# Kernel tuning notes

Hardware: AMD Instinct MI355X
Metric: run time of the kernel (lower is better)

Reference implementation:

```python
import jax, jax.numpy as jnp
import numpy as np
from jax.ops import segment_sum, segment_max

N, E, H, C = 20000, 320000, 4, 128
G, NF, EF, GF = 1024, 9, 4, 50
EPS = 1e-5
NEG_SLOPE = 0.2


def setup_inputs() -> dict:
    key = jax.random.key(0)
    ks = jax.random.split(key, 16)
    inp = {
        'x': jax.random.normal(ks[0], (N, NF), jnp.float32),
        'edge_attr': jax.random.normal(ks[1], (E, EF), jnp.float32),
        'global_feat': jax.random.normal(ks[2], (G, GF), jnp.float32),
        'Wl1': jax.random.normal(ks[3], (NF, H * C), jnp.float32) * 0.1,
        'Wr1': jax.random.normal(ks[4], (NF, H * C), jnp.float32) * 0.1,
        'We1': jax.random.normal(ks[5], (EF, H * C), jnp.float32) * 0.1,
        'att1': jax.random.normal(ks[6], (H, C), jnp.float32) * 0.1,
        'b1': jax.random.normal(ks[7], (H * C,), jnp.float32) * 0.01,
        'gamma1': jnp.ones((H * C,), jnp.float32),
        'beta1': jnp.zeros((H * C,), jnp.float32),
        'mean1': jnp.zeros((H * C,), jnp.float32),
        'var1': jnp.ones((H * C,), jnp.float32),
        'Wl2': jax.random.normal(ks[8], (H * C, H * C), jnp.float32) * 0.05,
        'Wr2': jax.random.normal(ks[9], (H * C, H * C), jnp.float32) * 0.05,
        'We2': jax.random.normal(ks[10], (EF, H * C), jnp.float32) * 0.1,
        'att2': jax.random.normal(ks[11], (H, C), jnp.float32) * 0.1,
        'b2': jax.random.normal(ks[12], (H * C,), jnp.float32) * 0.01,
        'gamma2': jnp.ones((H * C,), jnp.float32),
        'beta2': jnp.zeros((H * C,), jnp.float32),
        'mean2': jnp.zeros((H * C,), jnp.float32),
        'var2': jnp.ones((H * C,), jnp.float32),
        'fc1_w': jax.random.normal(ks[13], (H * C + GF, C), jnp.float32) * 0.05,
        'fc1_b': jnp.zeros((C,), jnp.float32),
        'fc2_w': jax.random.normal(ks[14], (C, 1), jnp.float32) * 0.1,
        'fc2_b': jnp.zeros((1,), jnp.float32),
        'edge_index': jax.random.randint(ks[15], (2, E), 0, N, jnp.int32),
        'batch': jnp.sort(jax.random.randint(jax.random.fold_in(key, 99), (N,), 0, G, jnp.int32)),
    }
    return inp


def gatv2_layer(x, src, dst, ea, Wl, Wr, We, att, bias):
    # PyG GATv2Conv: add self-loops with fill_value='mean' edge_attr
    n = x.shape[0]
    loop = jnp.arange(n, dtype=src.dtype)
    deg = segment_sum(jnp.ones((src.shape[0],), x.dtype), dst, num_segments=n)
    ea_mean = segment_sum(ea, dst, num_segments=n) / jnp.clip(deg, 1.0)[:, None]
    s = jnp.concatenate([src, loop])
    d = jnp.concatenate([dst, loop])
    eat = jnp.concatenate([ea, ea_mean], axis=0)
    xl = (x @ Wl).reshape(n, H, C)  # source transform
    xr = (x @ Wr).reshape(n, H, C)  # target transform
    ee = (eat @ We).reshape(-1, H, C)
    e = jax.nn.leaky_relu(xl[s] + xr[d] + ee, NEG_SLOPE)  # [E+N, H, C]
    logits = jnp.einsum('ehc,hc->eh', e, att)  # [E+N, H]
    m = segment_max(logits, d, num_segments=n)  # stable segment softmax
    ex = jnp.exp(logits - m[d])
    alpha = ex / segment_sum(ex, d, num_segments=n)[d]
    out = segment_sum(alpha[..., None] * xl[s], d, num_segments=n)  # [N, H, C]
    return out.reshape(n, H * C) + bias


def batch_norm(x, g, b, mu, var):
    return (x - mu) * jax.lax.rsqrt(var + EPS) * g + b


def reference(x, edge_attr, global_feat, Wl1, Wr1, We1, att1, b1, gamma1, beta1, mean1, var1,
              Wl2, Wr2, We2, att2, b2, gamma2, beta2, mean2, var2,
              fc1_w, fc1_b, fc2_w, fc2_b, edge_index, batch):
    src, dst = edge_index[0], edge_index[1]
    h = jax.nn.relu(batch_norm(gatv2_layer(x, src, dst, edge_attr, Wl1, Wr1, We1, att1, b1),
                               gamma1, beta1, mean1, var1))
    h = jax.nn.relu(batch_norm(gatv2_layer(h, src, dst, edge_attr, Wl2, Wr2, We2, att2, b2),
                               gamma2, beta2, mean2, var2))
    cnt = segment_sum(jnp.ones((h.shape[0],), h.dtype), batch, num_segments=G)
    pooled = segment_sum(h, batch, num_segments=G) / jnp.clip(cnt, 1.0)[:, None]  # [G, H*C]
    z = jnp.concatenate([pooled, global_feat], axis=1)
    z = jax.nn.relu(z @ fc1_w + fc1_b)
    return (z @ fc2_w + fc2_b).squeeze()
```

## Files before the change

kernel.cpp:

```cpp
#include <hip/hip_runtime.h>
#include <hip/hip_bf16.h>

#define Nn 20000
#define Ee 320000
#define Hh 4
#define Cc 128
#define HC 512
#define Gg 1024
#define NFt 9
#define EFt 4
#define GFt 50
#define EPSf 1e-5f
#define SLOPE 0.2f
#define NWAVES 4096

typedef __attribute__((ext_vector_type(8))) short bf16x8;
typedef __attribute__((ext_vector_type(4))) float f32x4;
typedef __attribute__((ext_vector_type(2))) float f32x2;
typedef __attribute__((ext_vector_type(4))) unsigned ui32x4;

typedef const __attribute__((address_space(1))) unsigned char* gp1_t;
typedef __attribute__((address_space(3))) unsigned char* lp3_t;
__device__ __forceinline__ void gload16(const void* g, void* l) {
    __builtin_amdgcn_global_load_lds((gp1_t)g, (lp3_t)l, 16, 0, 0);
}

__device__ __forceinline__ float bf2f(short s) {
    return __uint_as_float(((unsigned)(unsigned short)s) << 16);
}
__device__ __forceinline__ float rfl(float v) {
    return __uint_as_float(__builtin_amdgcn_readfirstlane(__float_as_uint(v)));
}

__device__ __forceinline__ f32x2 pkfma(f32x2 a, f32x2 b, f32x2 c) {
    f32x2 d;
    asm("v_pk_fma_f32 %0, %1, %2, %3" : "=v"(d) : "v"(a), "v"(b), "v"(c));
    return d;
}
__device__ __forceinline__ f32x2 pkadd(f32x2 a, f32x2 b) {
    f32x2 d;
    asm("v_pk_add_f32 %0, %1, %2" : "=v"(d) : "v"(a), "v"(b));
    return d;
}
__device__ __forceinline__ f32x2 pkmul(f32x2 a, f32x2 b) {
    f32x2 d;
    asm("v_pk_mul_f32 %0, %1, %2" : "=v"(d) : "v"(a), "v"(b));
    return d;
}

__global__ __launch_bounds__(256) void k_setup(
    const int* __restrict__ dst, int* __restrict__ deg, int* __restrict__ rank,
    const int* __restrict__ batch, int* __restrict__ gofs,
    const float* __restrict__ Wl2, const float* __restrict__ Wr2,
    __hip_bfloat16* __restrict__ Wt,
    const float* __restrict__ x, const float* __restrict__ Wl1,
    const float* __restrict__ Wr1, __hip_bfloat16* __restrict__ xl,
    __hip_bfloat16* __restrict__ xr) {
    __shared__ float tile[64][65];
    int b = blockIdx.x, t = threadIdx.x;
    if (b < 1250) {
        int e = b * 256 + t;
        if (e < Ee) rank[e] = atomicAdd(&deg[dst[e]], 1);
    } else if (b < 1329) {
        int i = (b - 1250) * 256 + t;
        if (i >= Nn) return;
        int bb = batch[i];
        if (i == 0) {
            for (int g = 0; g <= bb; ++g) gofs[g] = 0;
        } else {
            int bp = batch[i - 1];
            for (int g = bp + 1; g <= bb; ++g) gofs[g] = i;
        }
        if (i == Nn - 1) {
            for (int g = bb + 1; g <= Gg; ++g) gofs[g] = Nn;
        }
    } else if (b < 1457) {
        int tid = b - 1329;
        int tc = (tid >> 3) * 64;
        int tk = (tid & 7) * 64;
        int lc = t & 63, lr = t >> 6;
        const float* W = (tc < 512) ? Wl2 : Wr2;
        int cb = tc & 511;
#pragma unroll
        for (int i = 0; i < 16; ++i) {
            int r = lr * 16 + i;
            tile[r][lc] = W[(size_t)(tk + r) * 512 + cb + lc];
        }
        __syncthreads();
#pragma unroll
        for (int i = 0; i < 16; ++i) {
            int c = lr * 16 + i;
            Wt[(size_t)(tc + c) * 512 + tk + lc] = __float2bfloat16(tile[lc][c]);
        }
    } else {
        int l = t & 63, w = t >> 6;
        int ch0 = l * 8;
        int wid = (b - 1457) * 4 + w;
        int n0 = wid * 2, n1 = n0 + 1;
        float xa[NFt], xb[NFt];
#pragma unroll
        for (int f = 0; f < NFt; ++f) {
            xa[f] = x[n0 * NFt + f];
            xb[f] = x[n1 * NFt + f];
        }
        float a0[8] = {}, r0[8] = {}, a1[8] = {}, r1[8] = {};
#pragma unroll
        for (int f = 0; f < NFt; ++f) {
            f32x4 wl0 = *(const f32x4*)&Wl1[f * HC + ch0];
            f32x4 wl1 = *(const f32x4*)&Wl1[f * HC + ch0 + 4];
            f32x4 wr0 = *(const f32x4*)&Wr1[f * HC + ch0];
            f32x4 wr1 = *(const f32x4*)&Wr1[f * HC + ch0 + 4];
#pragma unroll
            for (int k = 0; k < 4; ++k) {
                a0[k] = fmaf(xa[f], wl0[k], a0[k]);
                a0[k + 4] = fmaf(xa[f], wl1[k], a0[k + 4]);
                r0[k] = fmaf(xa[f], wr0[k], r0[k]);
                r0[k + 4] = fmaf(xa[f], wr1[k], r0[k + 4]);
                a1[k] = fmaf(xb[f], wl0[k], a1[k]);
                a1[k + 4] = fmaf(xb[f], wl1[k], a1[k + 4]);
                r1[k] = fmaf(xb[f], wr0[k], r1[k]);
                r1[k + 4] = fmaf(xb[f], wr1[k], r1[k + 4]);
            }
        }
        auto cvt8 = [](const float* v) {
            bf16x8 o;
#pragma unroll
            for (int k = 0; k < 8; ++k) {
                union { float f; unsigned u; } cv;
                cv.f = v[k];
                unsigned r = (cv.u + 0x7fff + ((cv.u >> 16) & 1)) >> 16;
                o[k] = (short)r;
            }
            return o;
        };
        *(bf16x8*)(xl + (size_t)n0 * HC + ch0) = cvt8(a0);
        *(bf16x8*)(xr + (size_t)n0 * HC + ch0) = cvt8(r0);
        *(bf16x8*)(xl + (size_t)n1 * HC + ch0) = cvt8(a1);
        *(bf16x8*)(xr + (size_t)n1 * HC + ch0) = cvt8(r1);
    }
}

__global__ void k_scan(const int* __restrict__ deg, int* __restrict__ rowptr) {
    __shared__ int sums[1024];
    int t = threadIdx.x;
    const int n = Nn;
    int chunk = (n + 1023) / 1024;
    int start = t * chunk;
    int lim = min(start + chunk, n);
    int s = 0;
    for (int i = start; i < lim; ++i) s += deg[i];
    sums[t] = s;
    __syncthreads();
    for (int off = 1; off < 1024; off <<= 1) {
        int v = (t >= off) ? sums[t - off] : 0;
        __syncthreads();
        sums[t] += v;
        __syncthreads();
    }
    int run = (t == 0) ? 0 : sums[t - 1];
    for (int i = start; i < lim; ++i) { rowptr[i] = run; run += deg[i]; }
    if (t == 1023) rowptr[n] = sums[1023];
}

__global__ void k_scatter(const int* __restrict__ src, const int* __restrict__ dst,
                          const float* __restrict__ ea, const int* __restrict__ rowptr,
                          const int* __restrict__ rank, int* __restrict__ csr_src,
                          float4* __restrict__ ea_s) {
    int e = blockIdx.x * 256 + threadIdx.x;
    if (e >= Ee) return;
    int pos = rowptr[dst[e]] + rank[e];
    csr_src[pos] = src[e];
    ea_s[pos] = ((const float4*)ea)[e];
}

__global__ __launch_bounds__(256) void k_gemm_mfma(const short* __restrict__ Abf,
                                                   const short* __restrict__ Bt,
                                                   __hip_bfloat16* __restrict__ xl,
                                                   __hip_bfloat16* __restrict__ xr, int M) {
    __shared__ short As[128 * 32];
    __shared__ short Bs[128 * 32];
    int tid = threadIdx.x;
    int l = tid & 63;
    int wid = tid >> 6;
    int bm0 = blockIdx.x * 128;
    int bn0 = blockIdx.y * 128;
    int wr = (wid >> 1) * 64;
    int wc = (wid & 1) * 64;
    f32x4 acc[4][4] = {};

    int srow = l >> 2;
    int skoff = ((l & 3) ^ ((l >> 3) & 3)) * 8;
    int rk = (((l >> 4) ^ (l >> 1)) & 3) * 8;

    for (int k0 = 0; k0 < 512; k0 += 32) {
        {
            int c = wid;
            long row = min(bm0 + c * 16 + srow, M - 1);
            gload16(Abf + row * 512 + k0 + skoff, &As[c * 512]);
            int col = bn0 + c * 16 + srow;
            gload16(Bt + (size_t)col * 512 + k0 + skoff, &Bs[c * 512]);
            c = wid + 4;
            row = min(bm0 + c * 16 + srow, M - 1);
            gload16(Abf + row * 512 + k0 + skoff, &As[c * 512]);
            col = bn0 + c * 16 + srow;
            gload16(Bt + (size_t)col * 512 + k0 + skoff, &Bs[c * 512]);
        }
        asm volatile("s_waitcnt vmcnt(0)" ::: "memory");
        __syncthreads();
        bf16x8 af[4], bfr[4];
#pragma unroll
        for (int m = 0; m < 4; ++m)
            af[m] = *(const bf16x8*)&As[(wr + m * 16 + (l & 15)) * 32 + rk];
#pragma unroll
        for (int n = 0; n < 4; ++n)
            bfr[n] = *(const bf16x8*)&Bs[(wc + n * 16 + (l & 15)) * 32 + rk];
#pragma unroll
        for (int m = 0; m < 4; ++m)
#pragma unroll
            for (int n = 0; n < 4; ++n)
                acc[m][n] = __builtin_amdgcn_mfma_f32_16x16x32_bf16(af[m], bfr[n],
                                                                    acc[m][n], 0, 0, 0);
        __syncthreads();
    }
    __hip_bfloat16* dst = (bn0 < 512) ? xl : xr;
    int cb = bn0 & 511;
#pragma unroll
    for (int m = 0; m < 4; ++m) {
#pragma unroll
        for (int n = 0; n < 4; ++n) {
            int col = cb + wc + n * 16 + (l & 15);
#pragma unroll
            for (int r = 0; r < 4; ++r) {
                int row = bm0 + wr + m * 16 + (l >> 4) * 4 + r;
                if (row < M) dst[(size_t)row * 512 + col] = __float2bfloat16(acc[m][n][r]);
            }
        }
    }
}

__global__ __launch_bounds__(256) void k_fused_attn(
    const __hip_bfloat16* __restrict__ xl, const __hip_bfloat16* __restrict__ xr,
    const float* __restrict__ We, const float* __restrict__ att,
    const int* __restrict__ rowptr, const int* __restrict__ csr_src,
    const float4* __restrict__ ea_s, const float* __restrict__ bias,
    const float* __restrict__ gamma, const float* __restrict__ beta,
    const float* __restrict__ mean, const float* __restrict__ var,
    __hip_bfloat16* __restrict__ hout) {
    int l = threadIdx.x & 63;
    int wid = __builtin_amdgcn_readfirstlane(blockIdx.x * 4 + (threadIdx.x >> 6));
    int ch0 = l * 8;
    int nA = (int)(((long)wid * Nn) / NWAVES);
    int nB = (int)(((long)(wid + 1) * Nn) / NWAVES);

    f32x2 wee2[4][4], ar2[4];
#pragma unroll
    for (int f = 0; f < 4; ++f) {
        f32x4 w0 = *(const f32x4*)&We[f * HC + ch0];
        f32x4 w1 = *(const f32x4*)&We[f * HC + ch0 + 4];
        wee2[f][0] = (f32x2){w0.x, w0.y};
        wee2[f][1] = (f32x2){w0.z, w0.w};
        wee2[f][2] = (f32x2){w1.x, w1.y};
        wee2[f][3] = (f32x2){w1.z, w1.w};
    }
    {
        f32x4 a0 = *(const f32x4*)&att[ch0];
        f32x4 a1 = *(const f32x4*)&att[ch0 + 4];
        ar2[0] = (f32x2){a0.x, a0.y};
        ar2[1] = (f32x2){a0.z, a0.w};
        ar2[2] = (f32x2){a1.x, a1.y};
        ar2[3] = (f32x2){a1.z, a1.w};
    }
    float S[8], O[8];
    {
        f32x4 bi0 = *(const f32x4*)&bias[ch0], bi1 = *(const f32x4*)&bias[ch0 + 4];
        f32x4 ga0 = *(const f32x4*)&gamma[ch0], ga1 = *(const f32x4*)&gamma[ch0 + 4];
        f32x4 be0 = *(const f32x4*)&beta[ch0], be1 = *(const f32x4*)&beta[ch0 + 4];
        f32x4 me0 = *(const f32x4*)&mean[ch0], me1 = *(const f32x4*)&mean[ch0 + 4];
        f32x4 va0 = *(const f32x4*)&var[ch0], va1 = *(const f32x4*)&var[ch0 + 4];
#pragma unroll
        for (int k = 0; k < 8; ++k) {
            float bik = (k < 4) ? bi0[k] : bi1[k - 4];
            float gak = (k < 4) ? ga0[k] : ga1[k - 4];
            float bek = (k < 4) ? be0[k] : be1[k - 4];
            float mek = (k < 4) ? me0[k] : me1[k - 4];
            float vak = (k < 4) ? va0[k] : va1[k - 4];
            S[k] = gak * rsqrtf(vak + EPSf);
            O[k] = (bik - mek) * S[k] + bek;
        }
    }

    for (int n = nA; n < nB; ++n) {
        f32x2 rr2[4];
        {
            ui32x4 ru = *(const ui32x4*)(xr + (size_t)n * HC + ch0);
#pragma unroll
            for (int j = 0; j < 4; ++j) {
                unsigned u = ru[j];
                rr2[j] = (f32x2){__uint_as_float(u << 16),
                                 __uint_as_float(u & 0xffff0000u)};
            }
        }
        int start = __builtin_amdgcn_readfirstlane(rowptr[n]);
        int nedge = __builtin_amdgcn_readfirstlane(rowptr[n + 1]) - start;
        int last = start + nedge - 1;

        float m = -1e30f, den = 0.f;
        f32x2 acc2[4] = {};
        float es0 = 0.f, es1 = 0.f, es2 = 0.f, es3 = 0.f;

        struct Chunk {
            int s[4];
            float e[4][4];
            bf16x8 x[4];
        };

        auto accum4 = [&](const Chunk& c, const float* ex) {
#pragma unroll
            for (int i = 0; i < 4; ++i) {
                f32x2 esp = (f32x2){ex[i], ex[i]};
                ui32x4 xu = *(const ui32x4*)&c.x[i];
#pragma unroll
                for (int j = 0; j < 4; ++j) {
                    unsigned u = xu[j];
                    f32x2 xv = (f32x2){__uint_as_float(u << 16),
                                       __uint_as_float(u & 0xffff0000u)};
                    acc2[j] = pkfma(esp, xv, acc2[j]);
                }
            }
        };

        auto step = [&](Chunk& cur, Chunk& nxt, int base) {
#pragma unroll
            for (int i = 0; i < 4; ++i) {
                int idx = __builtin_amdgcn_readfirstlane(min(start + base + 4 + i, last));
                nxt.s[i] = __builtin_amdgcn_readfirstlane(csr_src[idx]);
                float4 v = ea_s[idx];
                nxt.e[i][0] = rfl(v.x); nxt.e[i][1] = rfl(v.y);
                nxt.e[i][2] = rfl(v.z); nxt.e[i][3] = rfl(v.w);
            }
#pragma unroll
            for (int i = 0; i < 4; ++i)
                nxt.x[i] = *(const bf16x8*)(xl + (size_t)nxt.s[i] * HC + ch0);

#pragma unroll
            for (int i = 0; i < 4; ++i) {
                if (base + i < nedge) {
                    es0 += cur.e[i][0]; es1 += cur.e[i][1];
                    es2 += cur.e[i][2]; es3 += cur.e[i][3];
                }
            }

            float p[4];
#pragma unroll
            for (int i = 0; i < 4; ++i) {
                ui32x4 xu = *(const ui32x4*)&cur.x[i];
                f32x2 es0p = (f32x2){cur.e[i][0], cur.e[i][0]};
                f32x2 es1p = (f32x2){cur.e[i][1], cur.e[i][1]};
                f32x2 es2p = (f32x2){cur.e[i][2], cur.e[i][2]};
                f32x2 es3p = (f32x2){cur.e[i][3], cur.e[i][3]};
                f32x2 plin = (f32x2){0.f, 0.f}, pabs = (f32x2){0.f, 0.f};
#pragma unroll
                for (int j = 0; j < 4; ++j) {
                    unsigned u = xu[j];
                    f32x2 xv = (f32x2){__uint_as_float(u << 16),
                                       __uint_as_float(u & 0xffff0000u)};
                    f32x2 z = pkadd(xv, rr2[j]);
                    z = pkfma(es0p, wee2[0][j], z);
                    z = pkfma(es1p, wee2[1][j], z);
                    z = pkfma(es2p, wee2[2][j], z);
                    z = pkfma(es3p, wee2[3][j], z);
                    f32x2 za = (f32x2){fabsf(z.x), fabsf(z.y)};
                    plin = pkfma(ar2[j], z, plin);
                    pabs = pkfma(ar2[j], za, pabs);
                }
                p[i] = 0.6f * (plin.x + plin.y) + 0.4f * (pabs.x + pabs.y);
            }
#pragma unroll
            for (int off = 8; off; off >>= 1) {
                p[0] += __shfl_xor(p[0], off);
                p[1] += __shfl_xor(p[1], off);
                p[2] += __shfl_xor(p[2], off);
                p[3] += __shfl_xor(p[3], off);
            }
#pragma unroll
            for (int i = 1; i < 4; ++i)
                if (base + i >= nedge) p[i] = -1e30f;

            float pmax = fmaxf(fmaxf(p[0], p[1]), fmaxf(p[2], p[3]));
            float ex[4];
            if (__all(pmax <= m + 8.f)) {
                ex[0] = __expf(p[0] - m); ex[1] = __expf(p[1] - m);
                ex[2] = __expf(p[2] - m); ex[3] = __expf(p[3] - m);
                den += ex[0] + ex[1] + ex[2] + ex[3];
                accum4(cur, ex);
            } else {
                float mn = fmaxf(m, pmax);
                float sc = __expf(m - mn);
                ex[0] = __expf(p[0] - mn); ex[1] = __expf(p[1] - mn);
                ex[2] = __expf(p[2] - mn); ex[3] = __expf(p[3] - mn);
                den = den * sc + ex[0] + ex[1] + ex[2] + ex[3];
                f32x2 scs = (f32x2){sc, sc};
#pragma unroll
                for (int j = 0; j < 4; ++j) acc2[j] = pkmul(acc2[j], scs);
                accum4(cur, ex);
                m = mn;
            }
        };

        if (nedge > 0) {
            Chunk A, B;
#pragma unroll
            for (int i = 0; i < 4; ++i) {
                int idx = __builtin_amdgcn_readfirstlane(min(start + i, last));
                A.s[i] = __builtin_amdgcn_readfirstlane(csr_src[idx]);
                float4 v = ea_s[idx];
                A.e[i][0] = rfl(v.x); A.e[i][1] = rfl(v.y);
                A.e[i][2] = rfl(v.z); A.e[i][3] = rfl(v.w);
            }
#pragma unroll
            for (int i = 0; i < 4; ++i)
                A.x[i] = *(const bf16x8*)(xl + (size_t)A.s[i] * HC + ch0);

            int base = 0;
            for (;;) {
                step(A, B, base);
                base += 4;
                if (base >= nedge) break;
                step(B, A, base);
                base += 4;
                if (base >= nedge) break;
            }
        }

        {
            float dv = (float)max(nedge, 1);
            float e0 = es0 / dv, e1 = es1 / dv, e2 = es2 / dv, e3 = es3 / dv;
            ui32x4 xu = *(const ui32x4*)(xl + (size_t)n * HC + ch0);
            f32x2 es0p = (f32x2){e0, e0}, es1p = (f32x2){e1, e1};
            f32x2 es2p = (f32x2){e2, e2}, es3p = (f32x2){e3, e3};
            f32x2 plin = (f32x2){0.f, 0.f}, pabs = (f32x2){0.f, 0.f};
            f32x2 xv2[4];
#pragma unroll
            for (int j = 0; j < 4; ++j) {
                unsigned u = xu[j];
                xv2[j] = (f32x2){__uint_as_float(u << 16),
                                 __uint_as_float(u & 0xffff0000u)};
                f32x2 z = pkadd(xv2[j], rr2[j]);
                z = pkfma(es0p, wee2[0][j], z);
                z = pkfma(es1p, wee2[1][j], z);
                z = pkfma(es2p, wee2[2][j], z);
                z = pkfma(es3p, wee2[3][j], z);
                f32x2 za = (f32x2){fabsf(z.x), fabsf(z.y)};
                plin = pkfma(ar2[j], z, plin);
                pabs = pkfma(ar2[j], za, pabs);
            }
            float pi = 0.6f * (plin.x + plin.y) + 0.4f * (pabs.x + pabs.y);
#pragma unroll
            for (int off = 8; off; off >>= 1) pi += __shfl_xor(pi, off);
            float mn = fmaxf(m, pi);
            float sc = __expf(m - mn);
            float ex = __expf(pi - mn);
            den = den * sc + ex;
            f32x2 scs = (f32x2){sc, sc};
            f32x2 exs = (f32x2){ex, ex};
#pragma unroll
            for (int j = 0; j < 4; ++j)
                acc2[j] = pkfma(exs, xv2[j], pkmul(acc2[j], scs));
        }

        float iden = 1.f / den;
        float aflat[8] = {acc2[0].x, acc2[0].y, acc2[1].x, acc2[1].y,
                          acc2[2].x, acc2[2].y, acc2[3].x, acc2[3].y};
        bf16x8 ob;
#pragma unroll
        for (int k = 0; k < 8; ++k) {
            float v = fmaxf(fmaf(aflat[k] * iden, S[k], O[k]), 0.f);
            union { float f; unsigned u; } cv;
            cv.f = v;
            unsigned r = (cv.u + 0x7fff + ((cv.u >> 16) & 1)) >> 16;
            ob[k] = (short)r;
        }
        *(bf16x8*)(hout + (size_t)n * HC + ch0) = ob;
    }
}

__global__ __launch_bounds__(256) void k_pool_mlp(
    const __hip_bfloat16* __restrict__ h, const int* __restrict__ gofs,
    const float* __restrict__ gfeat, const float* __restrict__ fc1w,
    const float* __restrict__ fc1b, const float* __restrict__ fc2w,
    const float* __restrict__ fc2b, float* __restrict__ out) {
    __shared__ float z[HC + GFt];
    __shared__ float red[256];
    int g = blockIdx.x, t = threadIdx.x;
    int s = gofs[g], e = gofs[g + 1];
    float a0 = 0.f, a1 = 0.f;
    for (int r = s; r < e; ++r) {
        ushort2 v = ((const ushort2*)(h + (size_t)r * HC))[t];
        a0 += bf2f((short)v.x);
        a1 += bf2f((short)v.y);
    }
    float ic = (e > s) ? 1.f / (float)(e - s) : 0.f;
    z[2 * t] = a0 * ic;
    z[2 * t + 1] = a1 * ic;
    if (t < GFt) z[HC + t] = gfeat[g * GFt + t];
    __syncthreads();
    int c = t & 127, half = t >> 7;
    float acc = (half == 0) ? fc1b[c] : 0.f;
    int j0 = half * 281, j1 = j0 + 281;
    for (int j = j0; j < j1; ++j) acc += z[j] * fc1w[j * 128 + c];
    red[t] = acc;
    __syncthreads();
    if (t < 128) {
        float a = red[t] + red[t + 128];
        red[t] = fmaxf(a, 0.f) * fc2w[t];
    }
    __syncthreads();
    for (int off = 64; off; off >>= 1) {
        if (t < off) red[t] += red[t + off];
        __syncthreads();
    }
    if (t == 0) out[g] = red[0] + fc2b[0];
}

extern "C" void kernel_launch(void* const* d_in, const int* in_sizes, int n_in,
                              void* d_out, int out_size, void* d_ws, size_t ws_size,
                              hipStream_t stream) {
    const float* x = (const float*)d_in[0];
    const float* ea = (const float*)d_in[1];
    const float* gfeat = (const float*)d_in[2];
    const float* Wl1 = (const float*)d_in[3];
    const float* Wr1 = (const float*)d_in[4];
    const float* We1 = (const float*)d_in[5];
    const float* att1 = (const float*)d_in[6];
    const float* b1 = (const float*)d_in[7];
    const float* gamma1 = (const float*)d_in[8];
    const float* beta1 = (const float*)d_in[9];
    const float* mean1 = (const float*)d_in[10];
    const float* var1 = (const float*)d_in[11];
    const float* Wl2 = (const float*)d_in[12];
    const float* Wr2 = (const float*)d_in[13];
    const float* We2 = (const float*)d_in[14];
    const float* att2 = (const float*)d_in[15];
    const float* b2 = (const float*)d_in[16];
    const float* gamma2 = (const float*)d_in[17];
    const float* beta2 = (const float*)d_in[18];
    const float* mean2 = (const float*)d_in[19];
    const float* var2 = (const float*)d_in[20];
    const float* fc1w = (const float*)d_in[21];
    const float* fc1b = (const float*)d_in[22];
    const float* fc2w = (const float*)d_in[23];
    const float* fc2b = (const float*)d_in[24];
    const int* eidx = (const int*)d_in[25];
    const int* batch = (const int*)d_in[26];
    float* out = (float*)d_out;

    const int* srcp = eidx;
    const int* dstp = eidx + Ee;

    char* p = (char*)d_ws;
    auto alloc = [&](size_t bytes) -> char* {
        char* r = p;
        p += (bytes + 255) & ~(size_t)255;
        return r;
    };
    __hip_bfloat16* xl = (__hip_bfloat16*)alloc((size_t)Nn * HC * 2);
    __hip_bfloat16* xr = (__hip_bfloat16*)alloc((size_t)Nn * HC * 2);
    __hip_bfloat16* h_bf = (__hip_bfloat16*)alloc((size_t)Nn * HC * 2);
    int* deg = (int*)alloc((size_t)Nn * 4);
    int* rank = (int*)alloc((size_t)Ee * 4);
    int* rowptr = (int*)alloc((size_t)(Nn + 1) * 4);
    int* csr_src = (int*)alloc((size_t)Ee * 4);
    float4* ea_s = (float4*)alloc((size_t)Ee * 16);
    int* gofs = (int*)alloc((size_t)(Gg + 1) * 4);
    __hip_bfloat16* Wt = (__hip_bfloat16*)alloc((size_t)1024 * 512 * 2);

    hipMemsetAsync(deg, 0, (size_t)Nn * 4, stream);

    k_setup<<<1457 + 2500, 256, 0, stream>>>(dstp, deg, rank, batch, gofs, Wl2, Wr2,
                                             Wt, x, Wl1, Wr1, xl, xr);
    k_scan<<<1, 1024, 0, stream>>>(deg, rowptr);
    k_scatter<<<(Ee + 255) / 256, 256, 0, stream>>>(srcp, dstp, ea, rowptr, rank,
                                                    csr_src, ea_s);

    k_fused_attn<<<NWAVES / 4, 256, 0, stream>>>(xl, xr, We1, att1, rowptr, csr_src,
                                                 ea_s, b1, gamma1, beta1, mean1, var1,
                                                 h_bf);

    k_gemm_mfma<<<dim3((Nn + 127) / 128, 8), 256, 0, stream>>>(
        (const short*)h_bf, (const short*)Wt, xl, xr, Nn);
    k_fused_attn<<<NWAVES / 4, 256, 0, stream>>>(xl, xr, We2, att2, rowptr, csr_src,
                                                 ea_s, b2, gamma2, beta2, mean2, var2,
                                                 h_bf);

    k_pool_mlp<<<Gg, 256, 0, stream>>>(h_bf, gofs, gfeat, fc1w, fc1b, fc2w, fc2b, out);
}
```

Measured before the change: 324.7 us.

## Assign one wave per node and stage edge metadata via lane bpermute

The attention kernel now launches one wave per destination node instead of a fixed pool of persistent waves that loop over node ranges. Each wave loads up to 64 edge source indices and edge attributes cooperatively, one per lane, and broadcasts them with ds_bpermute. This replaces the per-edge scalar readfirstlane loads. Gather addresses become 32-bit byte offsets, and the BN scale/offset is computed after the loop. The aim is to cut serialized scalar load latency and improve latency hiding across many waves, at the cost of more launched waves and recomputing per-wave constants for every node.

```diff
diff --git a/kernel.cpp b/kernel.cpp
--- a/kernel.cpp
+++ b/kernel.cpp
@@ -12,7 +12,6 @@
 #define GFt 50
 #define EPSf 1e-5f
 #define SLOPE 0.2f
-#define NWAVES 4096
 
 typedef __attribute__((ext_vector_type(8))) short bf16x8;
 typedef __attribute__((ext_vector_type(4))) float f32x4;
@@ -28,9 +27,6 @@
 __device__ __forceinline__ float bf2f(short s) {
     return __uint_as_float(((unsigned)(unsigned short)s) << 16);
 }
-__device__ __forceinline__ float rfl(float v) {
-    return __uint_as_float(__builtin_amdgcn_readfirstlane(__float_as_uint(v)));
-}
 
 __device__ __forceinline__ f32x2 pkfma(f32x2 a, f32x2 b, f32x2 c) {
     f32x2 d;
@@ -46,6 +42,12 @@
     f32x2 d;
     asm("v_pk_mul_f32 %0, %1, %2" : "=v"(d) : "v"(a), "v"(b));
     return d;
+}
+__device__ __forceinline__ int bperm(int byteaddr, int v) {
+    return __builtin_amdgcn_ds_bpermute(byteaddr, v);
+}
+__device__ __forceinline__ float bpermf(int byteaddr, float v) {
+    return __int_as_float(__builtin_amdgcn_ds_bpermute(byteaddr, __float_as_int(v)));
 }
 
 __global__ __launch_bounds__(256) void k_setup(
@@ -246,13 +248,14 @@
     const float* __restrict__ gamma, const float* __restrict__ beta,
     const float* __restrict__ mean, const float* __restrict__ var,
     __hip_bfloat16* __restrict__ hout) {
+    int n = blockIdx.x * 4 + (threadIdx.x >> 6);
+    if (n >= Nn) return;
     int l = threadIdx.x & 63;
-    int wid = __builtin_amdgcn_readfirstlane(blockIdx.x * 4 + (threadIdx.x >> 6));
     int ch0 = l * 8;
-    int nA = (int)(((long)wid * Nn) / NWAVES);
-    int nB = (int)(((long)(wid + 1) * Nn) / NWAVES);
-
-    f32x2 wee2[4][4], ar2[4];
+    const unsigned char* xlb = (const unsigned char*)xl;
+    int choff = ch0 * 2;
+
+    f32x2 wee2[4][4], ar2[4], rr2[4];
 #pragma unroll
     for (int f = 0; f < 4; ++f) {
         f32x4 w0 = *(const f32x4*)&We[f * HC + ch0];
@@ -270,55 +273,108 @@
         ar2[2] = (f32x2){a1.x, a1.y};
         ar2[3] = (f32x2){a1.z, a1.w};
     }
-    float S[8], O[8];
     {
-        f32x4 bi0 = *(const f32x4*)&bias[ch0], bi1 = *(const f32x4*)&bias[ch0 + 4];
-        f32x4 ga0 = *(const f32x4*)&gamma[ch0], ga1 = *(const f32x4*)&gamma[ch0 + 4];
-        f32x4 be0 = *(const f32x4*)&beta[ch0], be1 = *(const f32x4*)&beta[ch0 + 4];
-        f32x4 me0 = *(const f32x4*)&mean[ch0], me1 = *(const f32x4*)&mean[ch0 + 4];
-        f32x4 va0 = *(const f32x4*)&var[ch0], va1 = *(const f32x4*)&var[ch0 + 4];
-#pragma unroll
-        for (int k = 0; k < 8; ++k) {
-            float bik = (k < 4) ? bi0[k] : bi1[k - 4];
-            float gak = (k < 4) ? ga0[k] : ga1[k - 4];
-            float bek = (k < 4) ? be0[k] : be1[k - 4];
-            float mek = (k < 4) ? me0[k] : me1[k - 4];
-            float vak = (k < 4) ? va0[k] : va1[k - 4];
-            S[k] = gak * rsqrtf(vak + EPSf);
-            O[k] = (bik - mek) * S[k] + bek;
-        }
-    }
-
-    for (int n = nA; n < nB; ++n) {
-        f32x2 rr2[4];
-        {
-            ui32x4 ru = *(const ui32x4*)(xr + (size_t)n * HC + ch0);
+        ui32x4 ru = *(const ui32x4*)(xr + (size_t)n * HC + ch0);
+#pragma unroll
+        for (int j = 0; j < 4; ++j) {
+            unsigned u = ru[j];
+            rr2[j] = (f32x2){__uint_as_float(u << 16), __uint_as_float(u & 0xffff0000u)};
+        }
+    }
+
+    int start = __builtin_amdgcn_readfirstlane(rowptr[n]);
+    int nedge = __builtin_amdgcn_readfirstlane(rowptr[n + 1]) - start;
+
+    float m = -1e30f, den = 0.f;
+    f32x2 acc2[4] = {};
+    float esl0 = 0.f, esl1 = 0.f, esl2 = 0.f, esl3 = 0.f;
+
+    struct Chunk {
+        float e[4][4];
+        bf16x8 x[4];
+    };
+
+    for (int mb = 0; mb < nedge; mb += 64) {
+        int cnt = min(64, nedge - mb);
+        int msrc = 0;
+        float4 mea = make_float4(0.f, 0.f, 0.f, 0.f);
+        if (l < cnt) {
+            msrc = csr_src[start + mb + l];
+            mea = ea_s[start + mb + l];
+        }
+        esl0 += mea.x; esl1 += mea.y; esl2 += mea.z; esl3 += mea.w;
+
+        auto fetch = [&](Chunk& C, int fb) {
 #pragma unroll
             for (int j = 0; j < 4; ++j) {
-                unsigned u = ru[j];
-                rr2[j] = (f32x2){__uint_as_float(u << 16),
-                                 __uint_as_float(u & 0xffff0000u)};
-            }
-        }
-        int start = __builtin_amdgcn_readfirstlane(rowptr[n]);
-        int nedge = __builtin_amdgcn_readfirstlane(rowptr[n + 1]) - start;
-        int last = start + nedge - 1;
-
-        float m = -1e30f, den = 0.f;
-        f32x2 acc2[4] = {};
-        float es0 = 0.f, es1 = 0.f, es2 = 0.f, es3 = 0.f;
-
-        struct Chunk {
-            int s[4];
-            float e[4][4];
-            bf16x8 x[4];
+                int ba = min(fb + j, cnt - 1) * 4;
+                int sj = bperm(ba, msrc);
+                C.e[j][0] = bpermf(ba, mea.x);
+                C.e[j][1] = bpermf(ba, mea.y);
+                C.e[j][2] = bpermf(ba, mea.z);
+                C.e[j][3] = bpermf(ba, mea.w);
+                unsigned voff = ((unsigned)sj << 10) + choff;
+                C.x[j] = *(const bf16x8*)(xlb + voff);
+            }
         };
 
-        auto accum4 = [&](const Chunk& c, const float* ex) {
+        auto compute = [&](const Chunk& C, int base) {
+            float p[4];
+#pragma unroll
+            for (int i = 0; i < 4; ++i) {
+                ui32x4 xu = *(const ui32x4*)&C.x[i];
+                f32x2 e0p = (f32x2){C.e[i][0], C.e[i][0]};
+                f32x2 e1p = (f32x2){C.e[i][1], C.e[i][1]};
+                f32x2 e2p = (f32x2){C.e[i][2], C.e[i][2]};
+                f32x2 e3p = (f32x2){C.e[i][3], C.e[i][3]};
+                f32x2 plin = (f32x2){0.f, 0.f}, pabs = (f32x2){0.f, 0.f};
+#pragma unroll
+                for (int j = 0; j < 4; ++j) {
+                    unsigned u = xu[j];
+                    f32x2 xv = (f32x2){__uint_as_float(u << 16),
+                                       __uint_as_float(u & 0xffff0000u)};
+                    f32x2 z = pkadd(xv, rr2[j]);
+                    z = pkfma(e0p, wee2[0][j], z);
+                    z = pkfma(e1p, wee2[1][j], z);
+                    z = pkfma(e2p, wee2[2][j], z);
+                    z = pkfma(e3p, wee2[3][j], z);
+                    f32x2 za = (f32x2){fabsf(z.x), fabsf(z.y)};
+                    plin = pkfma(ar2[j], z, plin);
+                    pabs = pkfma(ar2[j], za, pabs);
+                }
+                p[i] = 0.6f * (plin.x + plin.y) + 0.4f * (pabs.x + pabs.y);
+            }
+#pragma unroll
+            for (int off = 8; off; off >>= 1) {
+                p[0] += __shfl_xor(p[0], off);
+                p[1] += __shfl_xor(p[1], off);
+                p[2] += __shfl_xor(p[2], off);
+                p[3] += __shfl_xor(p[3], off);
+            }
+#pragma unroll
+            for (int i = 1; i < 4; ++i)
+                if (base + i >= cnt) p[i] = -1e30f;
+
+            float pmax = fmaxf(fmaxf(p[0], p[1]), fmaxf(p[2], p[3]));
+            float ex[4];
+            float mloc = m;
+            if (!__all(pmax <= mloc + 8.f)) {
+                float mn = fmaxf(mloc, pmax);
+                float sc = __expf(mloc - mn);
+                den *= sc;
+                f32x2 scs = (f32x2){sc, sc};
+#pragma unroll
+                for (int j = 0; j < 4; ++j) acc2[j] = pkmul(acc2[j], scs);
+                m = mn;
+                mloc = mn;
+            }
+            ex[0] = __expf(p[0] - mloc); ex[1] = __expf(p[1] - mloc);
+            ex[2] = __expf(p[2] - mloc); ex[3] = __expf(p[3] - mloc);
+            den += ex[0] + ex[1] + ex[2] + ex[3];
 #pragma unroll
             for (int i = 0; i < 4; ++i) {
                 f32x2 esp = (f32x2){ex[i], ex[i]};
-                ui32x4 xu = *(const ui32x4*)&c.x[i];
+                ui32x4 xu = *(const ui32x4*)&C.x[i];
 #pragma unroll
                 for (int j = 0; j < 4; ++j) {
                     unsigned u = xu[j];
@@ -329,159 +385,88 @@
             }
         };
 
-        auto step = [&](Chunk& cur, Chunk& nxt, int base) {
-#pragma unroll
-            for (int i = 0; i < 4; ++i) {
-                int idx = __builtin_amdgcn_readfirstlane(min(start + base + 4 + i, last));
-                nxt.s[i] = __builtin_amdgcn_readfirstlane(csr_src[idx]);
-                float4 v = ea_s[idx];
-                nxt.e[i][0] = rfl(v.x); nxt.e[i][1] = rfl(v.y);
-                nxt.e[i][2] = rfl(v.z); nxt.e[i][3] = rfl(v.w);
-            }
-#pragma unroll
-            for (int i = 0; i < 4; ++i)
-                nxt.x[i] = *(const bf16x8*)(xl + (size_t)nxt.s[i] * HC + ch0);
-
-#pragma unroll
-            for (int i = 0; i < 4; ++i) {
-                if (base + i < nedge) {
-                    es0 += cur.e[i][0]; es1 += cur.e[i][1];
-                    es2 += cur.e[i][2]; es3 += cur.e[i][3];
-                }
-            }
-
-            float p[4];
-#pragma unroll
-            for (int i = 0; i < 4; ++i) {
-                ui32x4 xu = *(const ui32x4*)&cur.x[i];
-                f32x2 es0p = (f32x2){cur.e[i][0], cur.e[i][0]};
-                f32x2 es1p = (f32x2){cur.e[i][1], cur.e[i][1]};
-                f32x2 es2p = (f32x2){cur.e[i][2], cur.e[i][2]};
-                f32x2 es3p = (f32x2){cur.e[i][3], cur.e[i][3]};
-                f32x2 plin = (f32x2){0.f, 0.f}, pabs = (f32x2){0.f, 0.f};
-#pragma unroll
-                for (int j = 0; j < 4; ++j) {
-                    unsigned u = xu[j];
-                    f32x2 xv = (f32x2){__uint_as_float(u << 16),
-                                       __uint_as_float(u & 0xffff0000u)};
-                    f32x2 z = pkadd(xv, rr2[j]);
-                    z = pkfma(es0p, wee2[0][j], z);
-                    z = pkfma(es1p, wee2[1][j], z);
-                    z = pkfma(es2p, wee2[2][j], z);
-                    z = pkfma(es3p, wee2[3][j], z);
-                    f32x2 za = (f32x2){fabsf(z.x), fabsf(z.y)};
-                    plin = pkfma(ar2[j], z, plin);
-                    pabs = pkfma(ar2[j], za, pabs);
-                }
-                p[i] = 0.6f * (plin.x + plin.y) + 0.4f * (pabs.x + pabs.y);
-            }
-#pragma unroll
-            for (int off = 8; off; off >>= 1) {
-                p[0] += __shfl_xor(p[0], off);
-                p[1] += __shfl_xor(p[1], off);
-                p[2] += __shfl_xor(p[2], off);
-                p[3] += __shfl_xor(p[3], off);
-            }
-#pragma unroll
-            for (int i = 1; i < 4; ++i)
-                if (base + i >= nedge) p[i] = -1e30f;
-
-            float pmax = fmaxf(fmaxf(p[0], p[1]), fmaxf(p[2], p[3]));
-            float ex[4];
-            if (__all(pmax <= m + 8.f)) {
-                ex[0] = __expf(p[0] - m); ex[1] = __expf(p[1] - m);
-                ex[2] = __expf(p[2] - m); ex[3] = __expf(p[3] - m);
-                den += ex[0] + ex[1] + ex[2] + ex[3];
-                accum4(cur, ex);
-            } else {
-                float mn = fmaxf(m, pmax);
-                float sc = __expf(m - mn);
-                ex[0] = __expf(p[0] - mn); ex[1] = __expf(p[1] - mn);
-                ex[2] = __expf(p[2] - mn); ex[3] = __expf(p[3] - mn);
-                den = den * sc + ex[0] + ex[1] + ex[2] + ex[3];
-                f32x2 scs = (f32x2){sc, sc};
-#pragma unroll
-                for (int j = 0; j < 4; ++j) acc2[j] = pkmul(acc2[j], scs);
-                accum4(cur, ex);
-                m = mn;
-            }
-        };
-
-        if (nedge > 0) {
-            Chunk A, B;
-#pragma unroll
-            for (int i = 0; i < 4; ++i) {
-                int idx = __builtin_amdgcn_readfirstlane(min(start + i, last));
-                A.s[i] = __builtin_amdgcn_readfirstlane(csr_src[idx]);
-                float4 v = ea_s[idx];
-                A.e[i][0] = rfl(v.x); A.e[i][1] = rfl(v.y);
-                A.e[i][2] = rfl(v.z); A.e[i][3] = rfl(v.w);
-            }
-#pragma unroll
-            for (int i = 0; i < 4; ++i)
-                A.x[i] = *(const bf16x8*)(xl + (size_t)A.s[i] * HC + ch0);
-
-            int base = 0;
-            for (;;) {
-                step(A, B, base);
-                base += 4;
-                if (base >= nedge) break;
-                step(B, A, base);
-                base += 4;
-                if (base >= nedge) break;
-            }
-        }
-
-        {
-            float dv = (float)max(nedge, 1);
-            float e0 = es0 / dv, e1 = es1 / dv, e2 = es2 / dv, e3 = es3 / dv;
-            ui32x4 xu = *(const ui32x4*)(xl + (size_t)n * HC + ch0);
-            f32x2 es0p = (f32x2){e0, e0}, es1p = (f32x2){e1, e1};
-            f32x2 es2p = (f32x2){e2, e2}, es3p = (f32x2){e3, e3};
-            f32x2 plin = (f32x2){0.f, 0.f}, pabs = (f32x2){0.f, 0.f};
-            f32x2 xv2[4];
-#pragma unroll
-            for (int j = 0; j < 4; ++j) {
-                unsigned u = xu[j];
-                xv2[j] = (f32x2){__uint_as_float(u << 16),
-                                 __uint_as_float(u & 0xffff0000u)};
-                f32x2 z = pkadd(xv2[j], rr2[j]);
-                z = pkfma(es0p, wee2[0][j], z);
-                z = pkfma(es1p, wee2[1][j], z);
-                z = pkfma(es2p, wee2[2][j], z);
-                z = pkfma(es3p, wee2[3][j], z);
-                f32x2 za = (f32x2){fabsf(z.x), fabsf(z.y)};
-                plin = pkfma(ar2[j], z, plin);
-                pabs = pkfma(ar2[j], za, pabs);
-            }
-            float pi = 0.6f * (plin.x + plin.y) + 0.4f * (pabs.x + pabs.y);
-#pragma unroll
-            for (int off = 8; off; off >>= 1) pi += __shfl_xor(pi, off);
-            float mn = fmaxf(m, pi);
-            float sc = __expf(m - mn);
-            float ex = __expf(pi - mn);
-            den = den * sc + ex;
-            f32x2 scs = (f32x2){sc, sc};
-            f32x2 exs = (f32x2){ex, ex};
-#pragma unroll
-            for (int j = 0; j < 4; ++j)
-                acc2[j] = pkfma(exs, xv2[j], pkmul(acc2[j], scs));
-        }
-
-        float iden = 1.f / den;
-        float aflat[8] = {acc2[0].x, acc2[0].y, acc2[1].x, acc2[1].y,
-                          acc2[2].x, acc2[2].y, acc2[3].x, acc2[3].y};
-        bf16x8 ob;
-#pragma unroll
-        for (int k = 0; k < 8; ++k) {
-            float v = fmaxf(fmaf(aflat[k] * iden, S[k], O[k]), 0.f);
-            union { float f; unsigned u; } cv;
-            cv.f = v;
-            unsigned r = (cv.u + 0x7fff + ((cv.u >> 16) & 1)) >> 16;
-            ob[k] = (short)r;
-        }
-        *(bf16x8*)(hout + (size_t)n * HC + ch0) = ob;
-    }
+        Chunk A, B;
+        fetch(A, 0);
+        int base = 0;
+        for (;;) {
+            fetch(B, base + 4);
+            compute(A, base);
+            base += 4;
+            if (base >= cnt) break;
+            fetch(A, base + 4);
+            compute(B, base);
+            base += 4;
+            if (base >= cnt) break;
+        }
+    }
+
+    {
+#pragma unroll
+        for (int off = 32; off; off >>= 1) {
+            esl0 += __shfl_xor(esl0, off);
+            esl1 += __shfl_xor(esl1, off);
+            esl2 += __shfl_xor(esl2, off);
+            esl3 += __shfl_xor(esl3, off);
+        }
+        float dv = 1.f / (float)max(nedge, 1);
+        f32x2 e0p = (f32x2){esl0 * dv, esl0 * dv};
+        f32x2 e1p = (f32x2){esl1 * dv, esl1 * dv};
+        f32x2 e2p = (f32x2){esl2 * dv, esl2 * dv};
+        f32x2 e3p = (f32x2){esl3 * dv, esl3 * dv};
+        ui32x4 xu = *(const ui32x4*)(xl + (size_t)n * HC + ch0);
+        f32x2 plin = (f32x2){0.f, 0.f}, pabs = (f32x2){0.f, 0.f};
+        f32x2 xv2[4];
+#pragma unroll
+        for (int j = 0; j < 4; ++j) {
+            unsigned u = xu[j];
+            xv2[j] = (f32x2){__uint_as_float(u << 16), __uint_as_float(u & 0xffff0000u)};
+            f32x2 z = pkadd(xv2[j], rr2[j]);
+            z = pkfma(e0p, wee2[0][j], z);
+            z = pkfma(e1p, wee2[1][j], z);
+            z = pkfma(e2p, wee2[2][j], z);
+            z = pkfma(e3p, wee2[3][j], z);
+            f32x2 za = (f32x2){fabsf(z.x), fabsf(z.y)};
+            plin = pkfma(ar2[j], z, plin);
+            pabs = pkfma(ar2[j], za, pabs);
+        }
+        float pi = 0.6f * (plin.x + plin.y) + 0.4f * (pabs.x + pabs.y);
+#pragma unroll
+        for (int off = 8; off; off >>= 1) pi += __shfl_xor(pi, off);
+        float mn = fmaxf(m, pi);
+        float sc = __expf(m - mn);
+        float ex = __expf(pi - mn);
+        den = den * sc + ex;
+        f32x2 scs = (f32x2){sc, sc};
+        f32x2 exs = (f32x2){ex, ex};
+#pragma unroll
+        for (int j = 0; j < 4; ++j) acc2[j] = pkfma(exs, xv2[j], pkmul(acc2[j], scs));
+    }
+
+    float iden = 1.f / den;
+    f32x4 bi0 = *(const f32x4*)&bias[ch0], bi1 = *(const f32x4*)&bias[ch0 + 4];
+    f32x4 ga0 = *(const f32x4*)&gamma[ch0], ga1 = *(const f32x4*)&gamma[ch0 + 4];
+    f32x4 be0 = *(const f32x4*)&beta[ch0], be1 = *(const f32x4*)&beta[ch0 + 4];
+    f32x4 me0 = *(const f32x4*)&mean[ch0], me1 = *(const f32x4*)&mean[ch0 + 4];
+    f32x4 va0 = *(const f32x4*)&var[ch0], va1 = *(const f32x4*)&var[ch0 + 4];
+    float aflat[8] = {acc2[0].x, acc2[0].y, acc2[1].x, acc2[1].y,
+                      acc2[2].x, acc2[2].y, acc2[3].x, acc2[3].y};
+    bf16x8 ob;
+#pragma unroll
+    for (int k = 0; k < 8; ++k) {
+        float bik = (k < 4) ? bi0[k] : bi1[k - 4];
+        float gak = (k < 4) ? ga0[k] : ga1[k - 4];
+        float bek = (k < 4) ? be0[k] : be1[k - 4];
+        float mek = (k < 4) ? me0[k] : me1[k - 4];
+        float vak = (k < 4) ? va0[k] : va1[k - 4];
+        float Sk = gak * rsqrtf(vak + EPSf);
+        float Ok = (bik - mek) * Sk + bek;
+        float v = fmaxf(fmaf(aflat[k] * iden, Sk, Ok), 0.f);
+        union { float f; unsigned u; } cv;
+        cv.f = v;
+        unsigned r = (cv.u + 0x7fff + ((cv.u >> 16) & 1)) >> 16;
+        ob[k] = (short)r;
+    }
+    *(bf16x8*)(hout + (size_t)n * HC + ch0) = ob;
 }
 
 __global__ __launch_bounds__(256) void k_pool_mlp(
@@ -582,15 +567,15 @@
     k_scatter<<<(Ee + 255) / 256, 256, 0, stream>>>(srcp, dstp, ea, rowptr, rank,
                                                     csr_src, ea_s);
 
-    k_fused_attn<<<NWAVES / 4, 256, 0, stream>>>(xl, xr, We1, att1, rowptr, csr_src,
-                                                 ea_s, b1, gamma1, beta1, mean1, var1,
-                                                 h_bf);
+    k_fused_attn<<<(Nn + 3) / 4, 256, 0, stream>>>(xl, xr, We1, att1, rowptr, csr_src,
+                                                   ea_s, b1, gamma1, beta1, mean1,
+                                                   var1, h_bf);
 
     k_gemm_mfma<<<dim3((Nn + 127) / 128, 8), 256, 0, stream>>>(
         (const short*)h_bf, (const short*)Wt, xl, xr, Nn);
-    k_fused_attn<<<NWAVES / 4, 256, 0, stream>>>(xl, xr, We2, att2, rowptr, csr_src,
-                                                 ea_s, b2, gamma2, beta2, mean2, var2,
-                                                 h_bf);
+    k_fused_attn<<<(Nn + 3) / 4, 256, 0, stream>>>(xl, xr, We2, att2, rowptr, csr_src,
+                                                   ea_s, b2, gamma2, beta2, mean2,
+                                                   var2, h_bf);
 
     k_pool_mlp<<<Gg, 256, 0, stream>>>(h_bf, gofs, gfeat, fc1w, fc1b, fc2w, fc2b, out);
 }
```

Measured after the change: 330.4 us. No clear change (+1.8%).
